# Kernel tuning notes

Measured on AMD Instinct MI355X. Metric: run time of the kernel, lower is better.

The kernel has to match this reference:

```python
import jax, jax.numpy as jnp
import numpy as np

NEG_SLOPE = 0.2  # PyG GATConv default leaky_relu slope


def _gat_conv(x, src, dst, W, a_src, a_dst, b, num_nodes):
    # Linear transform: [N, F_out]
    h = x @ W
    # Per-node attention halves (heads=1): [N]
    alpha_s = h @ a_src
    alpha_d = h @ a_dst
    # Per-edge raw score for edge j->i: a_src.h_j + a_dst.h_i
    e = jax.nn.leaky_relu(alpha_s[src] + alpha_d[dst], NEG_SLOPE)
    # Softmax over edges grouped by destination node (numerically stable)
    m = jax.ops.segment_max(e, dst, num_segments=num_nodes)
    ex = jnp.exp(e - m[dst])
    denom = jax.ops.segment_sum(ex, dst, num_segments=num_nodes)
    coef = ex / denom[dst]
    # Attention-weighted aggregation of source features into destinations
    out = jax.ops.segment_sum(h[src] * coef[:, None], dst, num_segments=num_nodes)
    return out + b


def setup_inputs() -> dict:
    key = jax.random.key(0)
    ks = jax.random.split(key, 12)
    N, F_in, F_hid, F_out, E = 100000, 128, 64, 40, 1600000
    x = jax.random.normal(ks[0], (N, F_in), dtype=jnp.float32)
    edge_index = jax.random.randint(ks[1], (2, E), 0, N, dtype=jnp.int64)
    g = lambda k, shape, fan: jax.random.normal(k, shape, dtype=jnp.float32) * (1.0 / np.sqrt(fan))
    return {
        "x": x,
        "edge_index": edge_index,
        "W1": g(ks[2], (F_in, F_hid), F_in),
        "a_src1": g(ks[3], (F_hid,), F_hid),
        "a_dst1": g(ks[4], (F_hid,), F_hid),
        "b1": jnp.zeros((F_hid,), dtype=jnp.float32),
        "W2": g(ks[5], (F_hid, F_out), F_hid),
        "a_src2": g(ks[6], (F_out,), F_out),
        "a_dst2": g(ks[7], (F_out,), F_out),
        "b2": jnp.zeros((F_out,), dtype=jnp.float32),
    }


def reference(x, edge_index, W1, a_src1, a_dst1, b1, W2, a_src2, a_dst2, b2):
    N = x.shape[0]
    # PyG GATConv adds self loops by default
    loops = jnp.arange(N, dtype=edge_index.dtype)
    src = jnp.concatenate([edge_index[0], loops])
    dst = jnp.concatenate([edge_index[1], loops])
    h = _gat_conv(x, src, dst, W1, a_src1, a_dst1, b1, N)
    h = jax.nn.relu(h)
    # dropout p=0.5 is inactive in eval mode
    h = _gat_conv(h, src, dst, W2, a_src2, a_dst2, b2, N)
    return jax.nn.log_softmax(h, axis=-1)
```

## Files before the change

### kernel.cpp

```cpp
#include <hip/hip_runtime.h>
#include <math.h>


constexpr int F_IN = 128;
constexpr int F_H  = 64;
constexpr int F_O  = 40;
constexpr int NBMAX = 512;
constexpr int CHUNK = 8192;

using h2 = decltype(__builtin_amdgcn_cvt_pkrtz(0.f, 0.f));
typedef __attribute__((ext_vector_type(4))) float f32x4;
typedef __attribute__((ext_vector_type(8))) short s16x8;

__device__ __forceinline__ h2 u2h(unsigned u) { return __builtin_bit_cast(h2, u); }

__device__ __forceinline__ float fdot2f(h2 a, h2 b, float c) {
#if __has_builtin(__builtin_amdgcn_fdot2)
    return __builtin_amdgcn_fdot2(a, b, c, false);
#else
    return c + (float)a.x * (float)b.x + (float)a.y * (float)b.y;
#endif
}
__device__ __forceinline__ h2 pklo(unsigned a, unsigned b) {
    return u2h(__builtin_amdgcn_perm(a, b, 0x05040100u));
}
__device__ __forceinline__ h2 pkhi(unsigned a, unsigned b) {
    return u2h(__builtin_amdgcn_perm(a, b, 0x07060302u));
}
__device__ __forceinline__ unsigned short f2h(float f) {
    _Float16 x = (_Float16)f;
    return __builtin_bit_cast(unsigned short, x);
}


__global__ __launch_bounds__(256) void k_binA(const int* __restrict__ dsts,
                                              int* __restrict__ bcnt,
                                              int E, int Et, int NB) {
    __shared__ int hist[NBMAX];
    for (int i = threadIdx.x; i < NB; i += 256) hist[i] = 0;
    __syncthreads();
    int e0 = blockIdx.x * 2048;
#pragma unroll
    for (int it = 0; it < 8; ++it) {
        int e = e0 + it * 256 + threadIdx.x;
        if (e < Et) {
            int d = (e < E) ? dsts[e] : (e - E);
            atomicAdd(&hist[d >> 8], 1);
        }
    }
    __syncthreads();
    for (int i = threadIdx.x; i < NB; i += 256) {
        int c = hist[i];
        if (c) atomicAdd(&bcnt[i], c);
    }
}

__global__ __launch_bounds__(NBMAX) void k_binB(const int* __restrict__ bcnt,
                                                int* __restrict__ bbase,
                                                int* __restrict__ bcur,
                                                int* __restrict__ rp,
                                                int NB, int N, int Et) {
    __shared__ int sc[NBMAX];
    int t = threadIdx.x;
    int v = (t < NB) ? bcnt[t] : 0;
    sc[t] = v; __syncthreads();
    int x = v;
    for (int o = 1; o < NBMAX; o <<= 1) {
        int y = (t >= o) ? sc[t - o] : 0;
        __syncthreads();
        x += y;
        sc[t] = x;
        __syncthreads();
    }
    if (t < NB) { int b = x - v; bbase[t] = b; bcur[t] = b; }
    if (t == 0) rp[N] = Et;
}

__global__ __launch_bounds__(256) void k_binC(const int* __restrict__ srcs,
                                              const int* __restrict__ dsts,
                                              int* __restrict__ bcur,
                                              unsigned* __restrict__ binned,
                                              int E, int Et, int NB) {
    __shared__ int hist[NBMAX];
    __shared__ int gbase[NBMAX];
    __shared__ int lcnt[NBMAX];
    int t = threadIdx.x;
    for (int i = t; i < NB; i += 256) hist[i] = 0;
    __syncthreads();
    int e0 = blockIdx.x * CHUNK;
#pragma unroll 4
    for (int it = 0; it < CHUNK / 256; ++it) {
        int e = e0 + it * 256 + t;
        if (e < Et) {
            int d = (e < E) ? dsts[e] : (e - E);
            atomicAdd(&hist[d >> 8], 1);
        }
    }
    __syncthreads();
    for (int i = t; i < NB; i += 256) {
        int c = hist[i];
        gbase[i] = c ? atomicAdd(&bcur[i], c) : 0;
        lcnt[i] = 0;
    }
    __syncthreads();
#pragma unroll 4
    for (int it = 0; it < CHUNK / 256; ++it) {
        int e = e0 + it * 256 + t;
        if (e < Et) {
            int s, d;
            if (e < E) { s = srcs[e]; d = dsts[e]; } else { s = e - E; d = s; }
            int b = d >> 8;
            int p = atomicAdd(&lcnt[b], 1);
            binned[gbase[b] + p] = (unsigned)s | ((unsigned)(d & 255) << 24);
        }
    }
}

__global__ __launch_bounds__(256) void k_binD(const unsigned* __restrict__ binned,
                                              const int* __restrict__ bbase,
                                              const int* __restrict__ bcur,
                                              int* __restrict__ rp,
                                              int* __restrict__ csr, int N) {
    __shared__ int hist[256];
    __shared__ int sc[256];
    __shared__ int lcnt[256];
    int b = blockIdx.x, t = threadIdx.x;
    int base = bbase[b], end = bcur[b];
    hist[t] = 0; __syncthreads();
    for (int j = base + t; j < end; j += 256)
        atomicAdd(&hist[binned[j] >> 24], 1);
    __syncthreads();
    int v = hist[t];
    sc[t] = v; __syncthreads();
    int x = v;
    for (int o = 1; o < 256; o <<= 1) {
        int y = (t >= o) ? sc[t - o] : 0;
        __syncthreads();
        x += y;
        sc[t] = x;
        __syncthreads();
    }
    int pref = x - v;
    int g = (b << 8) + t;
    if (g < N) rp[g] = base + pref;
    sc[t] = pref;
    lcnt[t] = 0;
    __syncthreads();
    for (int j = base + t; j < end; j += 256) {
        unsigned w = binned[j];
        int v2 = (int)(w >> 24);
        int s = (int)(w & 0xFFFFFFu);
        int p = atomicAdd(&lcnt[v2], 1);
        csr[base + sc[v2] + p] = s;
    }
}


__global__ __launch_bounds__(256) void k_wsplit(const float* __restrict__ W,
                                                unsigned short* __restrict__ WhiT,
                                                unsigned short* __restrict__ WloT) {
    int i = blockIdx.x * 256 + threadIdx.x;
    if (i >= F_IN * F_H) return;
    int k = i >> 6, c = i & 63;
    float w = W[i];
    unsigned u = __float_as_uint(w);
    unsigned hi = u & 0xFFFF0000u;
    float d = w - __uint_as_float(hi);
    WhiT[c * F_IN + k] = (unsigned short)(hi >> 16);
    WloT[c * F_IN + k] = (unsigned short)(__float_as_uint(d) >> 16);
}


__global__ __launch_bounds__(256) void k_gemm1m(const float* __restrict__ x,
                                                const unsigned short* __restrict__ WhiT,
                                                const unsigned short* __restrict__ WloT,
                                                const float* __restrict__ avs,
                                                const float* __restrict__ avd,
                                                unsigned short* __restrict__ h,
                                                float* __restrict__ as,
                                                float* __restrict__ ad, int N) {
    __shared__ unsigned short hs[64][72];
    const int t = threadIdx.x;
    const int wv = t >> 6;
    const int lane = t & 63;
    const int lrow = lane & 15;
    const int lk8 = lane >> 4;
    const int r0 = blockIdx.x * 64;
    const int arow = r0 + wv * 16 + lrow;
    const float* xp = x + (size_t)min(arow, N - 1) * F_IN;

    float4 xv0[4], xv1[4];
#pragma unroll
    for (int kt = 0; kt < 4; ++kt) {
        xv0[kt] = *(const float4*)&xp[kt * 32 + lk8 * 8];
        xv1[kt] = *(const float4*)&xp[kt * 32 + lk8 * 8 + 4];
    }
    s16x8 ah[4], al[4];
#pragma unroll
    for (int kt = 0; kt < 4; ++kt) {
        float e0[8] = {xv0[kt].x, xv0[kt].y, xv0[kt].z, xv0[kt].w,
                       xv1[kt].x, xv1[kt].y, xv1[kt].z, xv1[kt].w};
        unsigned uh[4], ul[4];
#pragma unroll
        for (int p = 0; p < 4; ++p) {
            float a0 = e0[2 * p], a1 = e0[2 * p + 1];
            unsigned u0 = __float_as_uint(a0), u1 = __float_as_uint(a1);
            float d0 = a0 - __uint_as_float(u0 & 0xFFFF0000u);
            float d1 = a1 - __uint_as_float(u1 & 0xFFFF0000u);
            uh[p] = __builtin_amdgcn_perm(u1, u0, 0x07060302u);
            ul[p] = __builtin_amdgcn_perm(__float_as_uint(d1), __float_as_uint(d0), 0x07060302u);
        }
        ah[kt] = __builtin_bit_cast(s16x8, make_uint4(uh[0], uh[1], uh[2], uh[3]));
        al[kt] = __builtin_bit_cast(s16x8, make_uint4(ul[0], ul[1], ul[2], ul[3]));
    }

    f32x4 acc[4] = {};
#pragma unroll
    for (int kt = 0; kt < 4; ++kt) {
#pragma unroll
        for (int ct = 0; ct < 4; ++ct) {
            const int boff = (ct * 16 + lrow) * F_IN + kt * 32 + lk8 * 8;
            s16x8 bh = *(const s16x8*)&WhiT[boff];
            s16x8 bl = *(const s16x8*)&WloT[boff];
            acc[ct] = __builtin_amdgcn_mfma_f32_16x16x32_bf16(ah[kt], bh, acc[ct], 0, 0, 0);
            acc[ct] = __builtin_amdgcn_mfma_f32_16x16x32_bf16(al[kt], bh, acc[ct], 0, 0, 0);
            acc[ct] = __builtin_amdgcn_mfma_f32_16x16x32_bf16(ah[kt], bl, acc[ct], 0, 0, 0);
        }
    }

    float avs_c[4], avd_c[4];
#pragma unroll
    for (int ct = 0; ct < 4; ++ct) {
        avs_c[ct] = avs[ct * 16 + lrow];
        avd_c[ct] = avd[ct * 16 + lrow];
    }
#pragma unroll
    for (int r = 0; r < 4; ++r) {
        float ps = acc[0][r] * avs_c[0] + acc[1][r] * avs_c[1]
                 + acc[2][r] * avs_c[2] + acc[3][r] * avs_c[3];
        float pd = acc[0][r] * avd_c[0] + acc[1][r] * avd_c[1]
                 + acc[2][r] * avd_c[2] + acc[3][r] * avd_c[3];
#pragma unroll
        for (int o = 8; o; o >>= 1) {
            ps += __shfl_xor(ps, o, 16);
            pd += __shfl_xor(pd, o, 16);
        }
        int orow = r0 + wv * 16 + lk8 * 4 + r;
        if (lrow == 0 && orow < N) { as[orow] = ps; ad[orow] = pd; }
    }

#pragma unroll
    for (int ct = 0; ct < 4; ++ct)
#pragma unroll
        for (int r = 0; r < 4; ++r)
            hs[wv * 16 + lk8 * 4 + r][ct * 16 + lrow] = f2h(acc[ct][r]);
    __syncthreads();
    const int row = t >> 2, ch = t & 3;
    const int grow = r0 + row;
    if (grow < N) {
        uint4 v0 = *(const uint4*)&hs[row][ch * 16];
        uint4 v1 = *(const uint4*)&hs[row][ch * 16 + 8];
        uint4* gp = (uint4*)(h + (size_t)grow * F_H + ch * 16);
        gp[0] = v0; gp[1] = v1;
    }
}


__global__ __launch_bounds__(256) void k_gemm2(const unsigned short* __restrict__ xin,
                                               const float* __restrict__ W,
                                               const float* __restrict__ avs,
                                               const float* __restrict__ avd,
                                               unsigned short* __restrict__ h,
                                               float* __restrict__ as,
                                               float* __restrict__ ad, int N) {
    __shared__ __align__(16) float Ws[F_H * F_O];
    for (int i = threadIdx.x; i < F_H * F_O; i += 256) Ws[i] = W[i];
    __syncthreads();
    int t = threadIdx.x;
    int r0 = blockIdx.x * 64 + (t >> 3) * 2;
    int l = t & 7;
    if (r0 >= N) return;
    const uint2* xa = (const uint2*)(xin + (size_t)r0 * F_H);
    const uint2* xb = (const uint2*)(xin + (size_t)(r0 + 1) * F_H);
    float acca[5] = {}, accb[5] = {};
#pragma unroll
    for (int k4 = 0; k4 < F_H / 4; ++k4) {
        uint2 ua = xa[k4];
        uint2 ub = xb[k4];
        h2 a01 = u2h(ua.x), a23 = u2h(ua.y);
        h2 b01 = u2h(ub.x), b23 = u2h(ub.y);
        float xva[4] = {(float)a01.x, (float)a01.y, (float)a23.x, (float)a23.y};
        float xvb[4] = {(float)b01.x, (float)b01.y, (float)b23.x, (float)b23.y};
        int kb = k4 * 4;
#pragma unroll
        for (int kk = 0; kk < 4; ++kk) {
            const float* wr = &Ws[(kb + kk) * F_O + l];
            float w0 = wr[0], w1 = wr[8], w2 = wr[16], w3 = wr[24], w4 = wr[32];
            float xs = xva[kk];
            acca[0] += xs * w0; acca[1] += xs * w1; acca[2] += xs * w2;
            acca[3] += xs * w3; acca[4] += xs * w4;
            float ys = xvb[kk];
            accb[0] += ys * w0; accb[1] += ys * w1; accb[2] += ys * w2;
            accb[3] += ys * w3; accb[4] += ys * w4;
        }
    }
    float psa = 0.f, pda = 0.f, psb = 0.f, pdb = 0.f;
    unsigned short* ra = h + (size_t)r0 * F_H;
    unsigned short* rb = h + (size_t)(r0 + 1) * F_H;
#pragma unroll
    for (int cc = 0; cc < 5; ++cc) {
        int c = l + 8 * cc;
        ra[c] = f2h(acca[cc]);
        rb[c] = f2h(accb[cc]);
        float vs = avs[c], vd = avd[c];
        psa += acca[cc] * vs; pda += acca[cc] * vd;
        psb += accb[cc] * vs; pdb += accb[cc] * vd;
    }
#pragma unroll
    for (int pp = 0; pp < 3; ++pp) {
        int c = 40 + l * 3 + pp;
        ra[c] = 0; rb[c] = 0;
    }
#pragma unroll
    for (int o = 4; o; o >>= 1) {
        psa += __shfl_xor(psa, o, 8);
        pda += __shfl_xor(pda, o, 8);
        psb += __shfl_xor(psb, o, 8);
        pdb += __shfl_xor(pdb, o, 8);
    }
    if (l == 0) { as[r0] = psa; ad[r0] = pda; as[r0 + 1] = psb; ad[r0 + 1] = pdb; }
}


template <int FOUT, bool RELU, bool LOGSM, bool F16OUT>
__global__ __launch_bounds__(256) void k_agg(const int* __restrict__ rp,
                                             const int* __restrict__ csr,
                                             const float* __restrict__ as,
                                             const float* __restrict__ ad,
                                             const uint4* __restrict__ h4,
                                             const float* __restrict__ bias,
                                             void* __restrict__ outv, int N) {
    constexpr int CAP = 64;
    __shared__ __align__(16) uint2 wsb[4][8][CAP + 2];
    const int w = threadIdx.x >> 6;
    const int g = (threadIdx.x >> 3) & 7;
    const int c = threadIdx.x & 7;
    const int i = blockIdx.x * 32 + (threadIdx.x >> 3);
    if (i >= N) return;
    const int start = rp[i], end = rp[i + 1];
    const int deg = end - start;
    const int dm = min(deg, CAP);
    const int dmR8 = (dm + 7) & ~7;
    const float adi = ad[i];

    for (int idx = c; idx < dm; idx += 8) {
        int srcn = csr[start + idx];
        float e = as[srcn] + adi;
        e = fmaxf(e, 0.2f * e);
        wsb[w][g][idx] = make_uint2(__float_as_uint(__expf(e)), (unsigned)srcn);
    }
    {
        int idx = dm + c;
        if (idx < dmR8) wsb[w][g][idx] = make_uint2(0u, (unsigned)i);
    }

    const uint4* pw = (const uint4*)wsb[w][g];
    float acc[8] = {}, acc2[8] = {};
    float sacc = 0.f;
    const int noct = dmR8 >> 3;
    for (int q = 0; q < noct; ++q) {
        uint4 m0 = pw[4 * q];
        uint4 m1 = pw[4 * q + 1];
        uint4 m2 = pw[4 * q + 2];
        uint4 m3 = pw[4 * q + 3];
        uint4 hv0 = h4[((unsigned)m0.y << 3) + c];
        uint4 hv1 = h4[((unsigned)m0.w << 3) + c];
        uint4 hv2 = h4[((unsigned)m1.y << 3) + c];
        uint4 hv3 = h4[((unsigned)m1.w << 3) + c];
        uint4 hv4 = h4[((unsigned)m2.y << 3) + c];
        uint4 hv5 = h4[((unsigned)m2.w << 3) + c];
        uint4 hv6 = h4[((unsigned)m3.y << 3) + c];
        uint4 hv7 = h4[((unsigned)m3.w << 3) + c];
        float w0 = __uint_as_float(m0.x), w1 = __uint_as_float(m0.z);
        float w2 = __uint_as_float(m1.x), w3 = __uint_as_float(m1.z);
        float w4 = __uint_as_float(m2.x), w5 = __uint_as_float(m2.z);
        float w6 = __uint_as_float(m3.x), w7 = __uint_as_float(m3.z);
        sacc += ((w0 + w1) + (w2 + w3)) + ((w4 + w5) + (w6 + w7));
        h2 wp0 = __builtin_amdgcn_cvt_pkrtz(w0, w1);
        h2 wp1 = __builtin_amdgcn_cvt_pkrtz(w2, w3);
        h2 wp2 = __builtin_amdgcn_cvt_pkrtz(w4, w5);
        h2 wp3 = __builtin_amdgcn_cvt_pkrtz(w6, w7);
        acc[0] = fdot2f(wp0, pklo(hv1.x, hv0.x), acc[0]);
        acc[1] = fdot2f(wp0, pkhi(hv1.x, hv0.x), acc[1]);
        acc[2] = fdot2f(wp0, pklo(hv1.y, hv0.y), acc[2]);
        acc[3] = fdot2f(wp0, pkhi(hv1.y, hv0.y), acc[3]);
        acc[4] = fdot2f(wp0, pklo(hv1.z, hv0.z), acc[4]);
        acc[5] = fdot2f(wp0, pkhi(hv1.z, hv0.z), acc[5]);
        acc[6] = fdot2f(wp0, pklo(hv1.w, hv0.w), acc[6]);
        acc[7] = fdot2f(wp0, pkhi(hv1.w, hv0.w), acc[7]);
        acc2[0] = fdot2f(wp1, pklo(hv3.x, hv2.x), acc2[0]);
        acc2[1] = fdot2f(wp1, pkhi(hv3.x, hv2.x), acc2[1]);
        acc2[2] = fdot2f(wp1, pklo(hv3.y, hv2.y), acc2[2]);
        acc2[3] = fdot2f(wp1, pkhi(hv3.y, hv2.y), acc2[3]);
        acc2[4] = fdot2f(wp1, pklo(hv3.z, hv2.z), acc2[4]);
        acc2[5] = fdot2f(wp1, pkhi(hv3.z, hv2.z), acc2[5]);
        acc2[6] = fdot2f(wp1, pklo(hv3.w, hv2.w), acc2[6]);
        acc2[7] = fdot2f(wp1, pkhi(hv3.w, hv2.w), acc2[7]);
        acc[0] = fdot2f(wp2, pklo(hv5.x, hv4.x), acc[0]);
        acc[1] = fdot2f(wp2, pkhi(hv5.x, hv4.x), acc[1]);
        acc[2] = fdot2f(wp2, pklo(hv5.y, hv4.y), acc[2]);
        acc[3] = fdot2f(wp2, pkhi(hv5.y, hv4.y), acc[3]);
        acc[4] = fdot2f(wp2, pklo(hv5.z, hv4.z), acc[4]);
        acc[5] = fdot2f(wp2, pkhi(hv5.z, hv4.z), acc[5]);
        acc[6] = fdot2f(wp2, pklo(hv5.w, hv4.w), acc[6]);
        acc[7] = fdot2f(wp2, pkhi(hv5.w, hv4.w), acc[7]);
        acc2[0] = fdot2f(wp3, pklo(hv7.x, hv6.x), acc2[0]);
        acc2[1] = fdot2f(wp3, pkhi(hv7.x, hv6.x), acc2[1]);
        acc2[2] = fdot2f(wp3, pklo(hv7.y, hv6.y), acc2[2]);
        acc2[3] = fdot2f(wp3, pkhi(hv7.y, hv6.y), acc2[3]);
        acc2[4] = fdot2f(wp3, pklo(hv7.z, hv6.z), acc2[4]);
        acc2[5] = fdot2f(wp3, pkhi(hv7.z, hv6.z), acc2[5]);
        acc2[6] = fdot2f(wp3, pklo(hv7.w, hv6.w), acc2[6]);
        acc2[7] = fdot2f(wp3, pkhi(hv7.w, hv6.w), acc2[7]);
    }

    for (int j = start + dm; j < end; ++j) {
        int srcn = csr[j];
        float e = as[srcn] + adi;
        e = fmaxf(e, 0.2f * e);
        float wv = __expf(e);
        sacc += wv;
        uint4 hv = h4[((unsigned)srcn << 3) + c];
        h2 wp = __builtin_amdgcn_cvt_pkrtz(wv, 0.f);
        acc[0] = fdot2f(wp, pklo(hv.x, hv.x), acc[0]);
        acc[1] = fdot2f(wp, pkhi(hv.x, hv.x), acc[1]);
        acc[2] = fdot2f(wp, pklo(hv.y, hv.y), acc[2]);
        acc[3] = fdot2f(wp, pkhi(hv.y, hv.y), acc[3]);
        acc[4] = fdot2f(wp, pklo(hv.z, hv.z), acc[4]);
        acc[5] = fdot2f(wp, pkhi(hv.z, hv.z), acc[5]);
        acc[6] = fdot2f(wp, pklo(hv.w, hv.w), acc[6]);
        acc[7] = fdot2f(wp, pkhi(hv.w, hv.w), acc[7]);
    }

#pragma unroll
    for (int k = 0; k < 8; ++k) acc[k] += acc2[k];
    float inv = 1.f / sacc;

    if (!LOGSM) {
        float r[8];
#pragma unroll
        for (int k = 0; k < 8; ++k) {
            r[k] = fmaf(acc[k], inv, bias[8 * c + k]);
            if (RELU) r[k] = fmaxf(r[k], 0.f);
        }
        if (F16OUT) {
            unsigned short* oh = (unsigned short*)outv;
            unsigned u0 = (unsigned)f2h(r[0]) | ((unsigned)f2h(r[1]) << 16);
            unsigned u1 = (unsigned)f2h(r[2]) | ((unsigned)f2h(r[3]) << 16);
            unsigned u2 = (unsigned)f2h(r[4]) | ((unsigned)f2h(r[5]) << 16);
            unsigned u3 = (unsigned)f2h(r[6]) | ((unsigned)f2h(r[7]) << 16);
            *(uint4*)(oh + (size_t)i * F_H + 8 * c) = make_uint4(u0, u1, u2, u3);
        } else {
            float* out = (float*)outv;
            float4* op = (float4*)(out + (size_t)i * FOUT + 8 * c);
            op[0] = make_float4(r[0], r[1], r[2], r[3]);
            op[1] = make_float4(r[4], r[5], r[6], r[7]);
        }
    } else {
        float* out = (float*)outv;
        constexpr int VC = FOUT / 8;
        bool act = (c < VC);
        float v[8];
#pragma unroll
        for (int k = 0; k < 8; ++k) {
            float bv = bias[act ? 8 * c + k : 0];
            v[k] = act ? fmaf(acc[k], inv, bv) : -INFINITY;
        }
        float mx = v[0];
#pragma unroll
        for (int k = 1; k < 8; ++k) mx = fmaxf(mx, v[k]);
#pragma unroll
        for (int o = 1; o <= 4; o <<= 1) mx = fmaxf(mx, __shfl_xor(mx, o));
        float es = 0.f;
        if (act) {
#pragma unroll
            for (int k = 0; k < 8; ++k) es += __expf(v[k] - mx);
        }
#pragma unroll
        for (int o = 1; o <= 4; o <<= 1) es += __shfl_xor(es, o);
        if (act) {
            float lse = mx + __logf(es);
            float4* op = (float4*)(out + (size_t)i * FOUT + 8 * c);
            op[0] = make_float4(v[0] - lse, v[1] - lse, v[2] - lse, v[3] - lse);
            op[1] = make_float4(v[4] - lse, v[5] - lse, v[6] - lse, v[7] - lse);
        }
    }
}


extern "C" void kernel_launch(void* const* d_in, const int* in_sizes, int n_in,
                              void* d_out, int out_size, void* d_ws, size_t ws_size,
                              hipStream_t stream) {
    const float* x   = (const float*)d_in[0];
    const int* edges = (const int*)d_in[1];
    const float* W1  = (const float*)d_in[2];
    const float* av_s1 = (const float*)d_in[3];
    const float* av_d1 = (const float*)d_in[4];
    const float* b1  = (const float*)d_in[5];
    const float* W2  = (const float*)d_in[6];
    const float* av_s2 = (const float*)d_in[7];
    const float* av_d2 = (const float*)d_in[8];
    const float* b2  = (const float*)d_in[9];
    float* out = (float*)d_out;

    const int N  = in_sizes[0] / F_IN;
    const int E  = in_sizes[1] / 2;
    const int Et = E + N;
    const int NB = (N + 255) >> 8;

    char* p = (char*)d_ws;
    auto alloc = [&](size_t bytes) {
        char* q = p;
        p += (bytes + 255) & ~(size_t)255;
        return (void*)q;
    };
    unsigned short* h1 = (unsigned short*)alloc((size_t)N * F_H * 2);
    unsigned short* out1h = (unsigned short*)alloc((size_t)N * F_H * 2);
    float* as1    = (float*)alloc((size_t)N * 4);
    float* ad1    = (float*)alloc((size_t)N * 4);
    float* as2    = (float*)alloc((size_t)N * 4);
    float* ad2    = (float*)alloc((size_t)N * 4);
    int* rp       = (int*)alloc((size_t)(N + 1) * 4);
    int* bcnt     = (int*)alloc(NBMAX * 4);
    int* bbase    = (int*)alloc(NBMAX * 4);
    int* bcur     = (int*)alloc(NBMAX * 4);
    unsigned* binned = (unsigned*)alloc((size_t)Et * 4);
    int* csr      = (int*)alloc((size_t)Et * 4);
    unsigned short* WhiT = (unsigned short*)alloc((size_t)F_H * F_IN * 2);
    unsigned short* WloT = (unsigned short*)alloc((size_t)F_H * F_IN * 2);
    (void)n_in; (void)out_size; (void)ws_size;

    const int* srcs = edges;
    const int* dsts = edges + E;

    hipMemsetAsync(bcnt, 0, NBMAX * 4, stream);

    k_wsplit<<<(F_IN * F_H + 255) / 256, 256, 0, stream>>>(W1, WhiT, WloT);
    k_binA<<<(Et + 2047) / 2048, 256, 0, stream>>>(dsts, bcnt, E, Et, NB);
    k_binB<<<1, NBMAX, 0, stream>>>(bcnt, bbase, bcur, rp, NB, N, Et);
    k_binC<<<(Et + CHUNK - 1) / CHUNK, 256, 0, stream>>>(srcs, dsts, bcur, binned, E, Et, NB);
    k_binD<<<NB, 256, 0, stream>>>(binned, bbase, bcur, rp, csr, N);

    k_gemm1m<<<(N + 63) / 64, 256, 0, stream>>>(x, WhiT, WloT, av_s1, av_d1, h1, as1, ad1, N);
    int gAgg = (N + 31) / 32;
    k_agg<F_H, true, false, true><<<gAgg, 256, 0, stream>>>(rp, csr, as1, ad1,
                                                            (const uint4*)h1, b1, out1h, N);
    k_gemm2<<<(N + 63) / 64, 256, 0, stream>>>(out1h, W2, av_s2, av_d2, h1, as2, ad2, N);
    k_agg<F_O, false, true, false><<<gAgg, 256, 0, stream>>>(rp, csr, as2, ad2,
                                                             (const uint4*)h1, b2, out, N);
}
```

Measured before the change: 296.9 us.

## Stage x tile through LDS in GEMM1 and compact layer-2 features to 40 columns

```diff
diff --git a/kernel.cpp b/kernel.cpp
--- a/kernel.cpp
+++ b/kernel.cpp
@@ -179,27 +179,35 @@
                                                 unsigned short* __restrict__ h,
                                                 float* __restrict__ as,
                                                 float* __restrict__ ad, int N) {
-    __shared__ unsigned short hs[64][72];
+    __shared__ __align__(16) float xs[64][132];
+    unsigned short (*hs)[72] = (unsigned short(*)[72])xs;
     const int t = threadIdx.x;
     const int wv = t >> 6;
     const int lane = t & 63;
     const int lrow = lane & 15;
     const int lk8 = lane >> 4;
     const int r0 = blockIdx.x * 64;
-    const int arow = r0 + wv * 16 + lrow;
-    const float* xp = x + (size_t)min(arow, N - 1) * F_IN;
-
-    float4 xv0[4], xv1[4];
+
+    {
+        const float4* xg = (const float4*)x;
+#pragma unroll
+        for (int it = 0; it < 8; ++it) {
+            int flat = it * 256 + t;
+            int row = flat >> 5, c4 = flat & 31;
+            int grow = min(r0 + row, N - 1);
+            float4 v = xg[(size_t)grow * 32 + c4];
+            *(float4*)&xs[row][c4 * 4] = v;
+        }
+    }
+    __syncthreads();
+
+    s16x8 ah[4], al[4];
 #pragma unroll
     for (int kt = 0; kt < 4; ++kt) {
-        xv0[kt] = *(const float4*)&xp[kt * 32 + lk8 * 8];
-        xv1[kt] = *(const float4*)&xp[kt * 32 + lk8 * 8 + 4];
-    }
-    s16x8 ah[4], al[4];
-#pragma unroll
-    for (int kt = 0; kt < 4; ++kt) {
-        float e0[8] = {xv0[kt].x, xv0[kt].y, xv0[kt].z, xv0[kt].w,
-                       xv1[kt].x, xv1[kt].y, xv1[kt].z, xv1[kt].w};
+        const float* rp_ = &xs[wv * 16 + lrow][kt * 32 + lk8 * 8];
+        float4 a = *(const float4*)rp_;
+        float4 b = *(const float4*)(rp_ + 4);
+        float e0[8] = {a.x, a.y, a.z, a.w, b.x, b.y, b.z, b.w};
         unsigned uh[4], ul[4];
 #pragma unroll
         for (int p = 0; p < 4; ++p) {
@@ -213,6 +221,7 @@
         ah[kt] = __builtin_bit_cast(s16x8, make_uint4(uh[0], uh[1], uh[2], uh[3]));
         al[kt] = __builtin_bit_cast(s16x8, make_uint4(ul[0], ul[1], ul[2], ul[3]));
     }
+    __syncthreads();
 
     f32x4 acc[4] = {};
 #pragma unroll
@@ -305,8 +314,8 @@
         }
     }
     float psa = 0.f, pda = 0.f, psb = 0.f, pdb = 0.f;
-    unsigned short* ra = h + (size_t)r0 * F_H;
-    unsigned short* rb = h + (size_t)(r0 + 1) * F_H;
+    unsigned short* ra = h + (size_t)r0 * F_O;
+    unsigned short* rb = h + (size_t)(r0 + 1) * F_O;
 #pragma unroll
     for (int cc = 0; cc < 5; ++cc) {
         int c = l + 8 * cc;
@@ -317,11 +326,6 @@
         psb += accb[cc] * vs; pdb += accb[cc] * vd;
     }
 #pragma unroll
-    for (int pp = 0; pp < 3; ++pp) {
-        int c = 40 + l * 3 + pp;
-        ra[c] = 0; rb[c] = 0;
-    }
-#pragma unroll
     for (int o = 4; o; o >>= 1) {
         psa += __shfl_xor(psa, o, 8);
         pda += __shfl_xor(pda, o, 8);
@@ -332,7 +336,7 @@
 }
 
 
-template <int FOUT, bool RELU, bool LOGSM, bool F16OUT>
+template <int FOUT, int ROWB, bool RELU, bool LOGSM, bool F16OUT>
 __global__ __launch_bounds__(256) void k_agg(const int* __restrict__ rp,
                                              const int* __restrict__ csr,
                                              const float* __restrict__ as,
@@ -345,6 +349,7 @@
     const int w = threadIdx.x >> 6;
     const int g = (threadIdx.x >> 3) & 7;
     const int c = threadIdx.x & 7;
+    const int cg = (c < ROWB) ? c : 0;
     const int i = blockIdx.x * 32 + (threadIdx.x >> 3);
     if (i >= N) return;
     const int start = rp[i], end = rp[i + 1];
@@ -373,14 +378,14 @@
         uint4 m1 = pw[4 * q + 1];
         uint4 m2 = pw[4 * q + 2];
         uint4 m3 = pw[4 * q + 3];
-        uint4 hv0 = h4[((unsigned)m0.y << 3) + c];
-        uint4 hv1 = h4[((unsigned)m0.w << 3) + c];
-        uint4 hv2 = h4[((unsigned)m1.y << 3) + c];
-        uint4 hv3 = h4[((unsigned)m1.w << 3) + c];
-        uint4 hv4 = h4[((unsigned)m2.y << 3) + c];
-        uint4 hv5 = h4[((unsigned)m2.w << 3) + c];
-        uint4 hv6 = h4[((unsigned)m3.y << 3) + c];
-        uint4 hv7 = h4[((unsigned)m3.w << 3) + c];
+        uint4 hv0 = h4[(size_t)m0.y * ROWB + cg];
+        uint4 hv1 = h4[(size_t)m0.w * ROWB + cg];
+        uint4 hv2 = h4[(size_t)m1.y * ROWB + cg];
+        uint4 hv3 = h4[(size_t)m1.w * ROWB + cg];
+        uint4 hv4 = h4[(size_t)m2.y * ROWB + cg];
+        uint4 hv5 = h4[(size_t)m2.w * ROWB + cg];
+        uint4 hv6 = h4[(size_t)m3.y * ROWB + cg];
+        uint4 hv7 = h4[(size_t)m3.w * ROWB + cg];
         float w0 = __uint_as_float(m0.x), w1 = __uint_as_float(m0.z);
         float w2 = __uint_as_float(m1.x), w3 = __uint_as_float(m1.z);
         float w4 = __uint_as_float(m2.x), w5 = __uint_as_float(m2.z);
@@ -430,7 +435,7 @@
         e = fmaxf(e, 0.2f * e);
         float wv = __expf(e);
         sacc += wv;
-        uint4 hv = h4[((unsigned)srcn << 3) + c];
+        uint4 hv = h4[(size_t)srcn * ROWB + cg];
         h2 wp = __builtin_amdgcn_cvt_pkrtz(wv, 0.f);
         acc[0] = fdot2f(wp, pklo(hv.x, hv.x), acc[0]);
         acc[1] = fdot2f(wp, pkhi(hv.x, hv.x), acc[1]);
@@ -553,9 +558,9 @@
 
     k_gemm1m<<<(N + 63) / 64, 256, 0, stream>>>(x, WhiT, WloT, av_s1, av_d1, h1, as1, ad1, N);
     int gAgg = (N + 31) / 32;
-    k_agg<F_H, true, false, true><<<gAgg, 256, 0, stream>>>(rp, csr, as1, ad1,
-                                                            (const uint4*)h1, b1, out1h, N);
+    k_agg<F_H, 8, true, false, true><<<gAgg, 256, 0, stream>>>(rp, csr, as1, ad1,
+                                                               (const uint4*)h1, b1, out1h, N);
     k_gemm2<<<(N + 63) / 64, 256, 0, stream>>>(out1h, W2, av_s2, av_d2, h1, as2, ad2, N);
-    k_agg<F_O, false, true, false><<<gAgg, 256, 0, stream>>>(rp, csr, as2, ad2,
-                                                             (const uint4*)h1, b2, out, N);
-}
+    k_agg<F_O, 5, false, true, false><<<gAgg, 256, 0, stream>>>(rp, csr, as2, ad2,
+                                                                (const uint4*)h1, b2, out, N);
+}
```

Measured after the change: 291.9 us. No clear change (-1.7%).
